# Kernel tuning notes

Hardware: AMD Instinct MI355X
Metric: run time of the kernel (lower is better)

The kernel has to match this reference:

```python
import jax, jax.numpy as jnp
import numpy as np

N = 50000  # num nodes

def _cheb_norm(edge_index, n):
    # PyG ChebConv sym normalization with default lambda_max=2.0:
    # scaled Laplacian L_hat = -D^{-1/2} A D^{-1/2} (diagonal cancels to 0)
    src, dst = edge_index[0], edge_index[1]
    deg = jax.ops.segment_sum(jnp.ones(src.shape[0], jnp.float32), src, num_segments=n)
    dinv = jnp.where(deg > 0, jax.lax.rsqrt(jnp.maximum(deg, 1.0)), 0.0)
    norm = -dinv[src] * dinv[dst]  # [E]
    return src, dst, norm

def _prop(x, src, dst, norm, n):
    # out[i] = sum_{(j->i)} norm_e * x[j]
    return jax.ops.segment_sum(norm[:, None] * x[src], dst, num_segments=n)

def _cheb_layer(x, src, dst, norm, W, b, n):
    # W: [K=3, in, out]; Tx0=x, Tx1=L_hat x, Tx2=2 L_hat Tx1 - Tx0
    tx0 = x
    tx1 = _prop(tx0, src, dst, norm, n)
    tx2 = 2.0 * _prop(tx1, src, dst, norm, n) - tx0
    return tx0 @ W[0] + tx1 @ W[1] + tx2 @ W[2] + b

def setup_inputs() -> dict:
    key = jax.random.key(0)
    ks = jax.random.split(key, 8)
    E = 800000
    v = jax.random.normal(ks[0], (N, 32), jnp.float32)
    edge_index = jax.random.randint(ks[1], (2, E), 0, N, dtype=jnp.int64)
    def glorot(k, shape):
        fan_in, fan_out = shape[1], shape[2]
        s = jnp.sqrt(6.0 / (fan_in + fan_out))
        return jax.random.uniform(k, shape, jnp.float32, -s, s)
    W1 = glorot(ks[2], (3, 32, 128));  b1 = jnp.zeros((128,), jnp.float32)
    W2 = glorot(ks[3], (3, 128, 256)); b2 = jnp.zeros((256,), jnp.float32)
    W3 = glorot(ks[4], (3, 256, 512)); b3 = jnp.zeros((512,), jnp.float32)
    return {"v": v, "edge_index": edge_index, "W1": W1, "b1": b1,
            "W2": W2, "b2": b2, "W3": W3, "b3": b3}

def reference(v, edge_index, W1, b1, W2, b2, W3, b3):
    n = v.shape[0]
    src, dst, norm = _cheb_norm(edge_index, n)
    x = jax.nn.relu(_cheb_layer(v, src, dst, norm, W1, b1, n))
    x = jax.nn.relu(_cheb_layer(x, src, dst, norm, W2, b2, n))
    x = jax.nn.relu(_cheb_layer(x, src, dst, norm, W3, b3, n))
    return x
```

## Files before the change

### kernel.cpp

```cpp
#include <hip/hip_runtime.h>
#include <hip/hip_bf16.h>


typedef __bf16 bf16x8 __attribute__((ext_vector_type(8)));
typedef float f32x4 __attribute__((ext_vector_type(4)));
typedef unsigned short ushort_t;

struct EdgeRec { int s; float w; };

__device__ inline float bf2f(ushort_t u) { return __builtin_bit_cast(float, (unsigned)u << 16); }
__device__ inline ushort_t f2bf(float f) { return __builtin_bit_cast(ushort_t, (__bf16)f); }

union U8 { int4 v; ushort_t u[8]; };

__device__ inline void gload16(const ushort_t* g, ushort_t* l) {
    __builtin_amdgcn_global_load_lds(
        (const __attribute__((address_space(1))) unsigned int*)g,
        (__attribute__((address_space(3))) unsigned int*)l, 16, 0, 0);
}

__global__ void count_kernel(const int* __restrict__ src, const int* __restrict__ dst,
                             int* __restrict__ cnt_src, int* __restrict__ cnt_dst, int E, int N) {
    int e = blockIdx.x * blockDim.x + threadIdx.x;
    if (e >= E) return;
    int s = src[e], d = dst[e];
    if ((unsigned)s < (unsigned)N) atomicAdd(&cnt_src[s], 1);
    if ((unsigned)d < (unsigned)N) atomicAdd(&cnt_dst[d], 1);
}

__global__ void dinv_kernel(const int* __restrict__ cnt_src, float* __restrict__ dinv, int N) {
    int i = blockIdx.x * blockDim.x + threadIdx.x;
    if (i >= N) return;
    int c = cnt_src[i];
    dinv[i] = (c > 0) ? rsqrtf((float)c) : 0.0f;
}

__global__ void blocksum_kernel(const int* __restrict__ cnt, int* __restrict__ bsum, int N) {
    int i = blockIdx.x * 256 + threadIdx.x;
    int v = (i < N) ? cnt[i] : 0;
#pragma unroll
    for (int off = 32; off >= 1; off >>= 1) v += __shfl_xor(v, off);
    __shared__ int ws[4];
    if ((threadIdx.x & 63) == 0) ws[threadIdx.x >> 6] = v;
    __syncthreads();
    if (threadIdx.x == 0) bsum[blockIdx.x] = ws[0] + ws[1] + ws[2] + ws[3];
}

__global__ void scanblock_kernel(const int* __restrict__ bsum, int* __restrict__ boff, int nb) {
    __shared__ int s[256];
    int t = threadIdx.x;
    int v = (t < nb) ? bsum[t] : 0;
    s[t] = v;
    __syncthreads();
#pragma unroll
    for (int off = 1; off < 256; off <<= 1) {
        int u = (t >= off) ? s[t - off] : 0;
        __syncthreads();
        s[t] += u;
        __syncthreads();
    }
    if (t < nb) boff[t] = s[t] - v;
}

__global__ void scatter_scan_kernel(const int* __restrict__ cnt, const int* __restrict__ boff,
                                    int* __restrict__ row_ptr, int* __restrict__ wofs, int N) {
    __shared__ int s[256];
    int t = threadIdx.x;
    int i = blockIdx.x * 256 + t;
    int v = (i < N) ? cnt[i] : 0;
    s[t] = v;
    __syncthreads();
#pragma unroll
    for (int off = 1; off < 256; off <<= 1) {
        int u = (t >= off) ? s[t - off] : 0;
        __syncthreads();
        s[t] += u;
        __syncthreads();
    }
    int run = boff[blockIdx.x] + s[t] - v;
    if (i < N) { row_ptr[i] = run; wofs[i] = run; }
    else if (i == N) row_ptr[N] = run;
}

__global__ void fill_kernel(const int* __restrict__ src, const int* __restrict__ dst,
                            const float* __restrict__ dinv, int* __restrict__ wofs,
                            EdgeRec* __restrict__ ep, int E, int N) {
    int e = blockIdx.x * blockDim.x + threadIdx.x;
    if (e >= E) return;
    int s = src[e], d = dst[e];
    if ((unsigned)s >= (unsigned)N || (unsigned)d >= (unsigned)N) return;
    int pos = atomicAdd(&wofs[d], 1);
    EdgeRec er; er.s = s; er.w = -dinv[s] * dinv[d];
    ep[pos] = er;
}

__global__ void convin_kernel(const float* __restrict__ v, ushort_t* __restrict__ txb, int N) {
    int id = blockIdx.x * blockDim.x + threadIdx.x;
    if (id >= N * 4) return;
    int node = id >> 2, c = (id & 3) << 3;
    const float* p = &v[(size_t)node * 32 + c];
    U8 o;
#pragma unroll
    for (int i = 0; i < 8; ++i) o.u[i] = f2bf(p[i]);
    *(int4*)&txb[(size_t)node * 96 + c] = o.v;
}

template <int F, int PASS>
__global__ __launch_bounds__(256) void prop_kernel(ushort_t* __restrict__ txb,
                                                   const int* __restrict__ row_ptr,
                                                   const EdgeRec* __restrict__ ep, int N) {
    constexpr int T = F / 8;
    constexpr int NPB = 256 / T;
    constexpr int RS = 3 * F;
    constexpr int SRC = (PASS == 1) ? 0 : F;
    int tf = threadIdx.x % T;
    int node = blockIdx.x * NPB + threadIdx.x / T;
    if (node >= N) return;
    int e0 = row_ptr[node], e1 = row_ptr[node + 1];
    int fo = tf * 8;
    float acc[8] = {};
    int e = e0;
    for (; e + 1 < e1; e += 2) {
        EdgeRec ea = ep[e], eb = ep[e + 1];
        U8 xa, xb2;
        xa.v  = *(const int4*)&txb[(size_t)ea.s * RS + SRC + fo];
        xb2.v = *(const int4*)&txb[(size_t)eb.s * RS + SRC + fo];
#pragma unroll
        for (int i = 0; i < 8; ++i) acc[i] += ea.w * bf2f(xa.u[i]);
#pragma unroll
        for (int i = 0; i < 8; ++i) acc[i] += eb.w * bf2f(xb2.u[i]);
    }
    if (e < e1) {
        EdgeRec ea = ep[e];
        U8 xa;
        xa.v = *(const int4*)&txb[(size_t)ea.s * RS + SRC + fo];
#pragma unroll
        for (int i = 0; i < 8; ++i) acc[i] += ea.w * bf2f(xa.u[i]);
    }
    U8 o;
    if (PASS == 1) {
#pragma unroll
        for (int i = 0; i < 8; ++i) o.u[i] = f2bf(acc[i]);
        *(int4*)&txb[(size_t)node * RS + F + fo] = o.v;
    } else {
        U8 x0;
        x0.v = *(const int4*)&txb[(size_t)node * RS + fo];
#pragma unroll
        for (int i = 0; i < 8; ++i) o.u[i] = f2bf(2.f * acc[i] - bf2f(x0.u[i]));
        *(int4*)&txb[(size_t)node * RS + 2 * F + fo] = o.v;
    }
}

__global__ void convw_kernel(const float* __restrict__ W, ushort_t* __restrict__ Wt, int K, int Nout) {
    int id = blockIdx.x * blockDim.x + threadIdx.x;
    if (id >= K * Nout) return;
    int n = id / K, k = id % K;
    Wt[id] = f2bf(W[(size_t)k * Nout + n]);
}

template <bool BF16OUT, int NY>
__global__ __launch_bounds__(256) void gemm_kernel(const ushort_t* __restrict__ A,
                                                   const ushort_t* __restrict__ Bt,
                                                   const float* __restrict__ bias,
                                                   void* __restrict__ outp,
                                                   int M, int K, int Nout, int ostride,
                                                   int nwg) {
    __shared__ ushort_t As[128 * 32];
    __shared__ ushort_t Bs[128 * 32];
    int tid = threadIdx.x;
    int orig = blockIdx.x;
    int q = nwg >> 3, r = nwg & 7;
    int xcd = orig & 7, m8 = orig >> 3;
    int t = (xcd < r ? xcd * (q + 1) : r * (q + 1) + (xcd - r) * q) + m8;
    int brow = (t / NY) * 128;
    int bcol = (t % NY) * 128;

    int lane = tid & 63, w = tid >> 6;
    int wr = w >> 1, wc = w & 1;
    int g = lane >> 4, lr = lane & 15;
    f32x4 acc[4][4] = {};

    int srow[2], scol[2];
#pragma unroll
    for (int p = 0; p < 2; ++p) {
        int row = (p * 4 + w) * 16 + (lane >> 2);
        srow[p] = row;
        scol[p] = ((lane & 3) ^ ((row >> 1) & 3)) * 8;
    }

    for (int kt = 0; kt < K; kt += 32) {
#pragma unroll
        for (int p = 0; p < 2; ++p) {
            int ar = brow + srow[p]; ar = ar < M ? ar : M - 1;
            gload16(&A[(size_t)ar * K + kt + scol[p]], &As[(p * 4 + w) * 512]);
            gload16(&Bt[(size_t)(bcol + srow[p]) * K + kt + scol[p]], &Bs[(p * 4 + w) * 512]);
        }
        __syncthreads();
        bf16x8 a[4], b[4];
#pragma unroll
        for (int m = 0; m < 4; ++m) {
            int row = wr * 64 + m * 16 + lr;
            a[m] = *(const bf16x8*)&As[row * 32 + ((g ^ ((row >> 1) & 3)) * 8)];
        }
#pragma unroll
        for (int n = 0; n < 4; ++n) {
            int row = wc * 64 + n * 16 + lr;
            b[n] = *(const bf16x8*)&Bs[row * 32 + ((g ^ ((row >> 1) & 3)) * 8)];
        }
#pragma unroll
        for (int m = 0; m < 4; ++m)
#pragma unroll
            for (int n = 0; n < 4; ++n)
                acc[m][n] = __builtin_amdgcn_mfma_f32_16x16x32_bf16(a[m], b[n], acc[m][n], 0, 0, 0);
        __syncthreads();
    }

#pragma unroll
    for (int m = 0; m < 4; ++m) {
        int grow_base = brow + wr * 64 + m * 16 + g * 4;
#pragma unroll
        for (int n = 0; n < 4; ++n) {
            int gcol = bcol + wc * 64 + n * 16 + lr;
            float bv = bias[gcol];
#pragma unroll
            for (int r2 = 0; r2 < 4; ++r2) {
                int grow = grow_base + r2;
                if (grow < M) {
                    float v2 = acc[m][n][r2] + bv;
                    v2 = v2 > 0.f ? v2 : 0.f;
                    if (BF16OUT)
                        ((ushort_t*)outp)[(size_t)grow * ostride + gcol] = f2bf(v2);
                    else
                        ((float*)outp)[(size_t)grow * ostride + gcol] = v2;
                }
            }
        }
    }
}

extern "C" void kernel_launch(void* const* d_in, const int* in_sizes, int n_in,
                              void* d_out, int out_size, void* d_ws, size_t ws_size,
                              hipStream_t stream) {
    const float* v  = (const float*)d_in[0];
    const int*   ei = (const int*)d_in[1];
    const float* W1 = (const float*)d_in[2];
    const float* b1 = (const float*)d_in[3];
    const float* W2 = (const float*)d_in[4];
    const float* b2 = (const float*)d_in[5];
    const float* W3 = (const float*)d_in[6];
    const float* b3 = (const float*)d_in[7];

    const int N = in_sizes[0] / 32;
    const int E = in_sizes[1] / 2;
    const int* src = ei;
    const int* dst = ei + E;

    char* ws = (char*)d_ws;
    size_t off = 0;
    auto alloc = [&](size_t bytes) {
        off = (off + 255) & ~(size_t)255;
        char* p = ws + off;
        off += bytes;
        return p;
    };
    EdgeRec*  ep      = (EdgeRec*)alloc((size_t)E * 8);
    int*      row_ptr = (int*)alloc((size_t)(N + 1) * 4);
    int*      wofs    = (int*)alloc((size_t)N * 4);
    int*      cnt_src = (int*)alloc((size_t)N * 4);
    int*      cnt_dst = (int*)alloc((size_t)N * 4);
    float*    dinv    = (float*)alloc((size_t)N * 4);
    int*      bsum    = (int*)alloc((size_t)256 * 4);
    int*      boff    = (int*)alloc((size_t)256 * 4);
    ushort_t* Wt      = (ushort_t*)alloc((size_t)512 * 768 * 2);
    ushort_t* txb3    = (ushort_t*)alloc((size_t)N * 768 * 2);
    ushort_t* txb1    = txb3;
    ushort_t* txb2    = (ushort_t*)d_out;
    float*    outF    = (float*)d_out;

    const int nb = (N + 255) / 256;

    hipMemsetAsync(cnt_src, 0, (size_t)N * 4, stream);
    hipMemsetAsync(cnt_dst, 0, (size_t)N * 4, stream);
    count_kernel<<<(E + 255) / 256, 256, 0, stream>>>(src, dst, cnt_src, cnt_dst, E, N);
    dinv_kernel<<<(N + 255) / 256, 256, 0, stream>>>(cnt_src, dinv, N);
    blocksum_kernel<<<nb, 256, 0, stream>>>(cnt_dst, bsum, N);
    scanblock_kernel<<<1, 256, 0, stream>>>(bsum, boff, nb);
    scatter_scan_kernel<<<nb, 256, 0, stream>>>(cnt_dst, boff, row_ptr, wofs, N);
    fill_kernel<<<(E + 255) / 256, 256, 0, stream>>>(src, dst, dinv, wofs, ep, E, N);

    const int mt = (N + 127) / 128;

    convin_kernel<<<(N * 4 + 255) / 256, 256, 0, stream>>>(v, txb1, N);
    prop_kernel<32, 1><<<(N + 63) / 64, 256, 0, stream>>>(txb1, row_ptr, ep, N);
    prop_kernel<32, 2><<<(N + 63) / 64, 256, 0, stream>>>(txb1, row_ptr, ep, N);
    convw_kernel<<<(96 * 128 + 255) / 256, 256, 0, stream>>>(W1, Wt, 96, 128);
    gemm_kernel<true, 1><<<mt * 1, 256, 0, stream>>>(txb1, Wt, b1, txb2, N, 96, 128, 384, mt * 1);

    prop_kernel<128, 1><<<(N + 15) / 16, 256, 0, stream>>>(txb2, row_ptr, ep, N);
    prop_kernel<128, 2><<<(N + 15) / 16, 256, 0, stream>>>(txb2, row_ptr, ep, N);
    convw_kernel<<<(384 * 256 + 255) / 256, 256, 0, stream>>>(W2, Wt, 384, 256);
    gemm_kernel<true, 2><<<mt * 2, 256, 0, stream>>>(txb2, Wt, b2, txb3, N, 384, 256, 768, mt * 2);

    prop_kernel<256, 1><<<(N + 7) / 8, 256, 0, stream>>>(txb3, row_ptr, ep, N);
    prop_kernel<256, 2><<<(N + 7) / 8, 256, 0, stream>>>(txb3, row_ptr, ep, N);
    convw_kernel<<<(768 * 512 + 255) / 256, 256, 0, stream>>>(W3, Wt, 768, 512);
    gemm_kernel<false, 4><<<mt * 4, 256, 0, stream>>>(txb3, Wt, b3, outF, N, 768, 512, 512, mt * 4);
}
```

Before: 478.5 us.

## Double-buffer GEMM LDS tiles and unroll propagation gather by four

The GEMM kernel now uses two LDS buffers so the global-to-LDS load for the next K tile is issued before computing on the current one, with one barrier per iteration instead of two. Row offsets and swizzled LDS addresses are also precomputed outside the loop. The sparse propagation kernel unrolls its edge loop by four to keep more independent gathers in flight. The changes double the GEMM's LDS footprint, which may lower occupancy, and raise register pressure in the propagation kernel.

```diff
diff --git a/kernel.cpp b/kernel.cpp
--- a/kernel.cpp
+++ b/kernel.cpp
@@ -120,17 +120,20 @@
     int fo = tf * 8;
     float acc[8] = {};
     int e = e0;
-    for (; e + 1 < e1; e += 2) {
-        EdgeRec ea = ep[e], eb = ep[e + 1];
-        U8 xa, xb2;
-        xa.v  = *(const int4*)&txb[(size_t)ea.s * RS + SRC + fo];
-        xb2.v = *(const int4*)&txb[(size_t)eb.s * RS + SRC + fo];
-#pragma unroll
-        for (int i = 0; i < 8; ++i) acc[i] += ea.w * bf2f(xa.u[i]);
-#pragma unroll
-        for (int i = 0; i < 8; ++i) acc[i] += eb.w * bf2f(xb2.u[i]);
-    }
-    if (e < e1) {
+    for (; e + 3 < e1; e += 4) {
+        EdgeRec er[4];
+        U8 x[4];
+#pragma unroll
+        for (int j = 0; j < 4; ++j) er[j] = ep[e + j];
+#pragma unroll
+        for (int j = 0; j < 4; ++j)
+            x[j].v = *(const int4*)&txb[(size_t)er[j].s * RS + SRC + fo];
+#pragma unroll
+        for (int j = 0; j < 4; ++j)
+#pragma unroll
+            for (int i = 0; i < 8; ++i) acc[i] += er[j].w * bf2f(x[j].u[i]);
+    }
+    for (; e < e1; ++e) {
         EdgeRec ea = ep[e];
         U8 xa;
         xa.v = *(const int4*)&txb[(size_t)ea.s * RS + SRC + fo];
@@ -165,8 +168,8 @@
                                                    void* __restrict__ outp,
                                                    int M, int K, int Nout, int ostride,
                                                    int nwg) {
-    __shared__ ushort_t As[128 * 32];
-    __shared__ ushort_t Bs[128 * 32];
+    __shared__ ushort_t As[2][128 * 32];
+    __shared__ ushort_t Bs[2][128 * 32];
     int tid = threadIdx.x;
     int orig = blockIdx.x;
     int q = nwg >> 3, r = nwg & 7;
@@ -188,31 +191,51 @@
         scol[p] = ((lane & 3) ^ ((row >> 1) & 3)) * 8;
     }
 
+    size_t abase[2], bbase[2];
+#pragma unroll
+    for (int p = 0; p < 2; ++p) {
+        int ar = brow + srow[p]; ar = ar < M ? ar : M - 1;
+        abase[p] = (size_t)ar * K + scol[p];
+        bbase[p] = (size_t)(bcol + srow[p]) * K + scol[p];
+    }
+
+    auto stage = [&](int buf, int kt) {
+#pragma unroll
+        for (int p = 0; p < 2; ++p) {
+            gload16(&A[abase[p] + kt], &As[buf][(p * 4 + w) * 512]);
+            gload16(&Bt[bbase[p] + kt], &Bs[buf][(p * 4 + w) * 512]);
+        }
+    };
+
+    int aoff[4], boff4[4];
+#pragma unroll
+    for (int m = 0; m < 4; ++m) {
+        int row = wr * 64 + m * 16 + lr;
+        aoff[m] = row * 32 + ((g ^ ((row >> 1) & 3)) * 8);
+    }
+#pragma unroll
+    for (int n = 0; n < 4; ++n) {
+        int row = wc * 64 + n * 16 + lr;
+        boff4[n] = row * 32 + ((g ^ ((row >> 1) & 3)) * 8);
+    }
+
+    stage(0, 0);
+    __syncthreads();
+    int cur = 0;
     for (int kt = 0; kt < K; kt += 32) {
-#pragma unroll
-        for (int p = 0; p < 2; ++p) {
-            int ar = brow + srow[p]; ar = ar < M ? ar : M - 1;
-            gload16(&A[(size_t)ar * K + kt + scol[p]], &As[(p * 4 + w) * 512]);
-            gload16(&Bt[(size_t)(bcol + srow[p]) * K + kt + scol[p]], &Bs[(p * 4 + w) * 512]);
-        }
-        __syncthreads();
+        if (kt + 32 < K) stage(cur ^ 1, kt + 32);
         bf16x8 a[4], b[4];
 #pragma unroll
-        for (int m = 0; m < 4; ++m) {
-            int row = wr * 64 + m * 16 + lr;
-            a[m] = *(const bf16x8*)&As[row * 32 + ((g ^ ((row >> 1) & 3)) * 8)];
-        }
-#pragma unroll
-        for (int n = 0; n < 4; ++n) {
-            int row = wc * 64 + n * 16 + lr;
-            b[n] = *(const bf16x8*)&Bs[row * 32 + ((g ^ ((row >> 1) & 3)) * 8)];
-        }
+        for (int m = 0; m < 4; ++m) a[m] = *(const bf16x8*)&As[cur][aoff[m]];
+#pragma unroll
+        for (int n = 0; n < 4; ++n) b[n] = *(const bf16x8*)&Bs[cur][boff4[n]];
 #pragma unroll
         for (int m = 0; m < 4; ++m)
 #pragma unroll
             for (int n = 0; n < 4; ++n)
                 acc[m][n] = __builtin_amdgcn_mfma_f32_16x16x32_bf16(a[m], b[n], acc[m][n], 0, 0, 0);
         __syncthreads();
+        cur ^= 1;
     }
 
 #pragma unroll
```

New measurement: 466.0 us. 2.6% less time.
